# Kernel optimization log

Measured on AMD Instinct MI355X. Metric: run time of the kernel, lower is better.

The kernel has to match this reference:

```python
import jax, jax.numpy as jnp
import numpy as np

H, DH = 16, 64  # heads, dim_head (inner_dim = 1024)
VARIANCE_CONSTANT = 1.0


def setup_inputs() -> dict:
    key = jax.random.key(0)
    ks = jax.random.split(key, 6)
    b, n, m, dim = 8, 4096, 64, 1024
    inner = H * DH
    x = jax.random.normal(ks[0], (b, n, dim), dtype=jnp.float32)
    latents = jax.random.normal(ks[1], (b, m, dim), dtype=jnp.float32)
    mask = jax.random.randint(ks[2], (b, n), 0, 2).astype(bool)  # True = masked out
    sd = 1.0 / np.sqrt(dim)
    Wq = jax.random.normal(ks[3], (inner, dim), dtype=jnp.float32) * sd
    Wkv = jax.random.normal(ks[4], (2 * inner, dim), dtype=jnp.float32) * sd
    Wout = jax.random.normal(ks[5], (dim, inner), dtype=jnp.float32) * sd
    return {"x": x, "latents": latents, "mask": mask, "Wq": Wq, "Wkv": Wkv, "Wout": Wout}


def _split_heads(t):  # b n (h d) -> b h n d
    b, n, _ = t.shape
    return t.reshape(b, n, H, DH).transpose(0, 2, 1, 3)


def reference(x, latents, mask, Wq, Wkv, Wout):
    b, n, dim = x.shape
    scale = DH ** -0.5
    q = latents @ Wq.T                      # b m inner
    k, v = jnp.split(x @ Wkv.T, 2, axis=-1)  # b n inner each
    q = _split_heads(q) * scale             # b h m d
    k = _split_heads(k)                     # b h n d
    v = _split_heads(v)
    sim = jnp.einsum('bhid,bhjd->bhij', q, k)  # b h m n
    max_neg = -jnp.finfo(sim.dtype).max
    sim = jnp.where(mask[:, None, None, :], max_neg, sim)
    sim_new = sim - jax.lax.stop_gradient(sim.max(axis=-1, keepdims=True))
    # cross-query (dim=-2) unbiased variance -> std over latents, shape b h n
    std = jnp.sqrt(jnp.var(sim_new, axis=-2, ddof=1) + 1e-4)
    std = jnp.where(mask[:, None, :], VARIANCE_CONSTANT, std)
    loss_variance = jnp.mean(jax.nn.relu(VARIANCE_CONSTANT - std))
    attn = jax.nn.softmax(sim_new, axis=-1)
    out = jnp.einsum('bhij,bhjd->bhid', attn, v)         # b h m d
    out = out.transpose(0, 2, 1, 3).reshape(b, -1, H * DH)  # b m inner
    out = out @ Wout.T                                    # b m dim
    return out, loss_variance
```

## Files before the change

### kernel.cpp

```cpp
#include <hip/hip_runtime.h>


using u16 = unsigned short;
typedef short bf16x8_t __attribute__((ext_vector_type(8)));
typedef float f32x4_t __attribute__((ext_vector_type(4)));

__device__ __forceinline__ u16 f2bf(float f) {
    union { float f; unsigned u; } v; v.f = f;
    unsigned r = v.u + 0x7fffu + ((v.u >> 16) & 1u);
    return (u16)(r >> 16);
}

template <typename T> __device__ __forceinline__ T cvt_out(float v);
template <> __device__ __forceinline__ float cvt_out<float>(float v) { return v; }
template <> __device__ __forceinline__ u16   cvt_out<u16>(float v)   { return f2bf(v); }

__device__ __forceinline__ void cp16(const void* g, void* l) {
    __builtin_amdgcn_global_load_lds((const __attribute__((address_space(1))) unsigned int*)g,
                                     (__attribute__((address_space(3))) unsigned int*)l, 16, 0, 0);
}

__global__ void cvt_all(const float* __restrict__ x, const float* __restrict__ lat,
                        const float* __restrict__ wq, const float* __restrict__ wkv,
                        const float* __restrict__ wout,
                        u16* __restrict__ xb, u16* __restrict__ latb,
                        u16* __restrict__ wqb, u16* __restrict__ wkvb,
                        u16* __restrict__ woutb) {
    int i = blockIdx.x * 256 + threadIdx.x;
    const float* s; u16* d; int off; float sc = 1.f;
    if (i < 8388608)      { s = x;    d = xb;    off = i; }
    else if (i < 8519680) { s = lat;  d = latb;  off = i - 8388608; }
    else if (i < 8781824) { s = wq;   d = wqb;   off = i - 8519680; sc = 0.125f; }
    else if (i < 9306112) { s = wkv;  d = wkvb;  off = i - 8781824; }
    else if (i < 9568256) { s = wout; d = woutb; off = i - 9306112; }
    else return;
    float4 v = ((const float4*)s)[off];
    ushort4 o;
    o.x = f2bf(v.x * sc); o.y = f2bf(v.y * sc);
    o.z = f2bf(v.z * sc); o.w = f2bf(v.w * sc);
    ((ushort4*)d)[off] = o;
}


__device__ __forceinline__ void stage_half(const u16* __restrict__ G, u16* L,
                                           int grow0, int kt, int tid) {
    const int row8 = tid >> 3;
    const int pcb = tid & 7;
    const int sc = (pcb ^ (row8 & 7)) * 8;
    const int k0 = kt * 64;
    const int wu = (tid >> 6) * 512;
#pragma unroll
    for (int r = 0; r < 2; ++r)
        cp16(G + (size_t)(grow0 + r * 64 + row8) * 1024 + k0 + sc, L + r * 4096 + wu);
}

template <bool E12, bool E34, int WAIT>
__device__ __forceinline__ void tile_phases(
    const u16* At, const u16* Bt,
    const u16* __restrict__ gA, u16* lA, int rowA, int ktA,
    const u16* __restrict__ gB, u16* lB, int rowB, int ktB,
    int wm, int wn, int frow, int pc0, int pc1, int tid,
    f32x4_t (&acc)[8][4]) {
    bf16x8_t aF[4][2], bF[4][2];
#pragma unroll
    for (int i = 0; i < 4; ++i) {
        const u16* p = At + (wm * 128 + i * 16 + frow) * 64;
        aF[i][0] = *(const bf16x8_t*)(p + pc0);
        aF[i][1] = *(const bf16x8_t*)(p + pc1);
    }
#pragma unroll
    for (int j = 0; j < 4; ++j)
        bF[j][0] = *(const bf16x8_t*)(Bt + (wn * 64 + j * 16 + frow) * 64 + pc0);
    if (E12) stage_half(gA, lA, rowA, ktA, tid);
    __builtin_amdgcn_s_barrier();
    asm volatile("s_waitcnt lgkmcnt(0)" ::: "memory");
    __builtin_amdgcn_s_setprio(1);
#pragma unroll
    for (int i = 0; i < 4; ++i)
#pragma unroll
        for (int j = 0; j < 4; ++j)
            acc[i][j] = __builtin_amdgcn_mfma_f32_16x16x32_bf16(aF[i][0], bF[j][0], acc[i][j], 0, 0, 0);
    __builtin_amdgcn_s_setprio(0);
    __builtin_amdgcn_s_barrier();
#pragma unroll
    for (int j = 0; j < 4; ++j)
        bF[j][1] = *(const bf16x8_t*)(Bt + (wn * 64 + j * 16 + frow) * 64 + pc1);
    if (E12) stage_half(gA, lA + 8192, rowA + 128, ktA, tid);
    __builtin_amdgcn_s_barrier();
    asm volatile("s_waitcnt lgkmcnt(0)" ::: "memory");
    __builtin_amdgcn_s_setprio(1);
#pragma unroll
    for (int i = 0; i < 4; ++i)
#pragma unroll
        for (int j = 0; j < 4; ++j)
            acc[i][j] = __builtin_amdgcn_mfma_f32_16x16x32_bf16(aF[i][1], bF[j][1], acc[i][j], 0, 0, 0);
    __builtin_amdgcn_s_setprio(0);
    __builtin_amdgcn_s_barrier();
#pragma unroll
    for (int i = 0; i < 4; ++i) {
        const u16* p = At + (wm * 128 + (i + 4) * 16 + frow) * 64;
        aF[i][0] = *(const bf16x8_t*)(p + pc0);
        aF[i][1] = *(const bf16x8_t*)(p + pc1);
    }
    if (E34) stage_half(gB, lB, rowB, ktB, tid);
    __builtin_amdgcn_s_barrier();
    asm volatile("s_waitcnt lgkmcnt(0)" ::: "memory");
    __builtin_amdgcn_s_setprio(1);
#pragma unroll
    for (int i = 0; i < 4; ++i)
#pragma unroll
        for (int j = 0; j < 4; ++j)
            acc[i + 4][j] = __builtin_amdgcn_mfma_f32_16x16x32_bf16(aF[i][0], bF[j][0], acc[i + 4][j], 0, 0, 0);
    __builtin_amdgcn_s_setprio(0);
    __builtin_amdgcn_s_barrier();
    if (E34) stage_half(gB, lB + 8192, rowB + 128, ktB, tid);
    if (WAIT == 4)      asm volatile("s_waitcnt vmcnt(4)" ::: "memory");
    else if (WAIT == 0) asm volatile("s_waitcnt vmcnt(0)" ::: "memory");
    __builtin_amdgcn_s_barrier();
    __builtin_amdgcn_s_setprio(1);
#pragma unroll
    for (int i = 0; i < 4; ++i)
#pragma unroll
        for (int j = 0; j < 4; ++j)
            acc[i + 4][j] = __builtin_amdgcn_mfma_f32_16x16x32_bf16(aF[i][1], bF[j][1], acc[i + 4][j], 0, 0, 0);
    __builtin_amdgcn_s_setprio(0);
    __builtin_amdgcn_s_barrier();
}

__global__ __launch_bounds__(512, 2) void gemm_kv8(const u16* __restrict__ A,
                                                   const u16* __restrict__ B,
                                                   const u16* __restrict__ Qb,
                                                   const int* __restrict__ mask,
                                                   u16* __restrict__ Kc,
                                                   u16* __restrict__ Vt,
                                                   float* __restrict__ Mg2) {
    __shared__ __align__(16) u16 smem[65536];
    u16* A0 = smem;
    u16* A1 = smem + 16384;
    u16* B0 = smem + 32768;
    u16* B1 = smem + 49152;
    const int tid = threadIdx.x;
    const int wid = tid >> 6, lane = tid & 63;
    const int wm = wid >> 2, wn = wid & 3;
    const int frow = lane & 15, fq = lane >> 4;
    const int pc0 = (fq ^ (frow & 7)) * 8;
    const int pc1 = ((4 + fq) ^ (frow & 7)) * 8;
    const int fid = blockIdx.x;
    const int xcd = fid & 7, l = fid >> 3;
    const int by = xcd * 16 + (l >> 3), bx = l & 7;
    const int bm = by * 256, bn = bx * 256;

    f32x4_t acc[8][4];
#pragma unroll
    for (int i = 0; i < 8; ++i)
#pragma unroll
        for (int j = 0; j < 4; ++j) acc[i][j] = (f32x4_t){0.f, 0.f, 0.f, 0.f};

    stage_half(B, B0, bn, 0, tid);        stage_half(B, B0 + 8192, bn + 128, 0, tid);
    stage_half(A, A0, bm, 0, tid);        stage_half(A, A0 + 8192, bm + 128, 0, tid);
    stage_half(B, B1, bn, 1, tid);        stage_half(B, B1 + 8192, bn + 128, 1, tid);
    asm volatile("s_waitcnt vmcnt(4)" ::: "memory");
    __builtin_amdgcn_s_barrier();

    for (int t = 0; t < 7; ++t) {
        tile_phases<true, true, 4>(A0, B0, A, A1, bm, 2 * t + 1, B, B0, bn, 2 * t + 2,
                                   wm, wn, frow, pc0, pc1, tid, acc);
        tile_phases<true, true, 4>(A1, B1, A, A0, bm, 2 * t + 2, B, B1, bn, 2 * t + 3,
                                   wm, wn, frow, pc0, pc1, tid, acc);
    }
    tile_phases<true, false, 0>(A0, B0, A, A1, bm, 15, B, B1, bn, 0,
                                wm, wn, frow, pc0, pc1, tid, acc);
    tile_phases<false, false, -1>(A1, B1, A, A0, bm, 0, B, B1, bn, 0,
                                  wm, wn, frow, pc0, pc1, tid, acc);

    if (bx < 4) {
        const int bb = bm >> 12, jb = bm & 4095, chunk = by & 15;
#pragma unroll
        for (int i = 0; i < 8; ++i)
#pragma unroll
            for (int j = 0; j < 4; ++j) {
                size_t base = (size_t)(bm + wm * 128 + i * 16 + fq * 4) * 1024 +
                              (bn + wn * 64 + j * 16 + frow);
#pragma unroll
                for (int r = 0; r < 4; ++r)
                    Kc[base + (size_t)r * 1024] = f2bf(acc[i][j][r]);
            }
        u16* Kl = smem;
#pragma unroll
        for (int i = 0; i < 8; ++i)
#pragma unroll
            for (int j = 0; j < 4; ++j) {
                const int cc0 = wn * 64 + j * 16 + frow;
#pragma unroll
                for (int r = 0; r < 4; ++r) {
                    const int jr = wm * 128 + i * 16 + fq * 4 + r;
                    Kl[jr * 256 + (((cc0 >> 3) ^ (jr & 7)) * 8) + (cc0 & 7)] = f2bf(acc[i][j][r]);
                }
            }
        __syncthreads();
        const int hh = wid >> 1, jn = (wid & 1) * 128;
        const int hc = (bx << 2) + hh;
        int mk[8];
#pragma unroll
        for (int jf = 0; jf < 8; ++jf)
            mk[jf] = mask[bb * 4096 + jb + jn + jf * 16 + frow];
        f32x4_t s2[4][8];
#pragma unroll
        for (int i = 0; i < 4; ++i)
#pragma unroll
            for (int jf = 0; jf < 8; ++jf) s2[i][jf] = (f32x4_t){0.f, 0.f, 0.f, 0.f};
#pragma unroll
        for (int ks = 0; ks < 2; ++ks) {
            bf16x8_t aq[4], bk[8];
#pragma unroll
            for (int i = 0; i < 4; ++i)
                aq[i] = *(const bf16x8_t*)(Qb + (size_t)(bb * 64 + i * 16 + frow) * 1024 +
                                           hc * 64 + ks * 32 + fq * 8);
#pragma unroll
            for (int jf = 0; jf < 8; ++jf) {
                const int jr = jn + jf * 16 + frow;
                bk[jf] = *(const bf16x8_t*)(Kl + jr * 256 +
                                            (((hh * 8 + ks * 4 + fq) ^ (jr & 7)) * 8));
            }
#pragma unroll
            for (int i = 0; i < 4; ++i)
#pragma unroll
                for (int jf = 0; jf < 8; ++jf)
                    s2[i][jf] = __builtin_amdgcn_mfma_f32_16x16x32_bf16(aq[i], bk[jf], s2[i][jf], 0, 0, 0);
        }
        float ml[16];
#pragma unroll
        for (int i = 0; i < 16; ++i) ml[i] = -3.0e38f;
#pragma unroll
        for (int jf = 0; jf < 8; ++jf)
            if (!mk[jf])
#pragma unroll
                for (int i = 0; i < 4; ++i)
#pragma unroll
                    for (int r = 0; r < 4; ++r)
                        ml[i * 4 + r] = fmaxf(ml[i * 4 + r], s2[i][jf][r]);
#pragma unroll
        for (int i = 0; i < 16; ++i) {
            float v = ml[i];
            v = fmaxf(v, __shfl_xor(v, 1)); v = fmaxf(v, __shfl_xor(v, 2));
            v = fmaxf(v, __shfl_xor(v, 4)); v = fmaxf(v, __shfl_xor(v, 8));
            ml[i] = v;
        }
        __syncthreads();
        float* Mp = (float*)smem;
        if ((lane & 15) == 0)
#pragma unroll
            for (int i = 0; i < 4; ++i)
#pragma unroll
                for (int r = 0; r < 4; ++r)
                    Mp[wid * 64 + i * 16 + fq * 4 + r] = ml[i * 4 + r];
        __syncthreads();
        if (tid < 256) {
            const int h2 = tid >> 6, m = tid & 63;
            Mg2[((size_t)(bb * 16 + (bx << 2) + h2) * 16 + chunk) * 64 + m] =
                fmaxf(Mp[(2 * h2) * 64 + m], Mp[(2 * h2 + 1) * 64 + m]);
        }
        return;
    }

    const int vb0 = bn - 1024;
    const int b = bm >> 12, jb = bm & 4095;
    u16* Ct = smem;
#pragma unroll
    for (int ph = 0; ph < 2; ++ph) {
        __syncthreads();
        if ((wn >> 1) == ph) {
#pragma unroll
            for (int i = 0; i < 8; ++i)
#pragma unroll
                for (int j = 0; j < 4; ++j) {
                    const int vdl = (wn & 1) * 64 + j * 16 + frow;
                    const int jl = wm * 128 + i * 16 + fq * 4;
                    ushort4 pk;
                    pk.x = f2bf(acc[i][j][0]); pk.y = f2bf(acc[i][j][1]);
                    pk.z = f2bf(acc[i][j][2]); pk.w = f2bf(acc[i][j][3]);
                    *(ushort4*)(Ct + vdl * 264 + jl) = pk;
                }
        }
        __syncthreads();
#pragma unroll
        for (int p = 0; p < 8; ++p) {
            const int idx = p * 512 + tid;
            const int vdl = idx >> 5;
            const int jl = (idx & 31) * 8;
            bf16x8_t v = *(const bf16x8_t*)(Ct + vdl * 264 + jl);
            const int vd = vb0 + ph * 128 + vdl;
            const size_t addr = ((size_t)(b * 16 + (vd >> 6)) * 64 + (vd & 63)) * 4096 + jb + jl;
            *(bf16x8_t*)(Vt + addr) = v;
        }
    }
}

template <typename OutT>
__global__ __launch_bounds__(256) void gemm_bt64(const u16* __restrict__ A,
                                                 const u16* __restrict__ B,
                                                 OutT* __restrict__ C,
                                                 int M, int N, int K) {
    __shared__ __align__(16) u16 As[64 * 64];
    __shared__ __align__(16) u16 Bs[64 * 64];
    const int tid = threadIdx.x;
    const int wid = tid >> 6, lane = tid & 63;
    const int bm = blockIdx.y * 64, bn = blockIdx.x * 64;
    const int srow = lane >> 3;
    const int scol = ((lane & 7) ^ srow) * 8;
    const int frow = lane & 15;
    const int wr = (wid >> 1) * 32, wc = (wid & 1) * 32;

    f32x4_t acc[2][2];
#pragma unroll
    for (int i = 0; i < 2; ++i)
#pragma unroll
        for (int j = 0; j < 2; ++j) acc[i][j] = (f32x4_t){0.f, 0.f, 0.f, 0.f};

    for (int k0 = 0; k0 < K; k0 += 64) {
#pragma unroll
        for (int t = 0; t < 2; ++t) {
            const int c = wid * 2 + t;
            const int r = c * 8 + srow;
            cp16(A + (size_t)(bm + r) * K + k0 + scol, As + c * 512);
            cp16(B + (size_t)(bn + r) * K + k0 + scol, Bs + c * 512);
        }
        __syncthreads();
#pragma unroll
        for (int ks = 0; ks < 2; ++ks) {
            const int grp = (((ks * 4 + (lane >> 4)) ^ (frow & 7)) * 8);
            bf16x8_t af[2], bfv[2];
#pragma unroll
            for (int i = 0; i < 2; ++i) {
                af[i]  = *(const bf16x8_t*)(As + (wr + i * 16 + frow) * 64 + grp);
                bfv[i] = *(const bf16x8_t*)(Bs + (wc + i * 16 + frow) * 64 + grp);
            }
#pragma unroll
            for (int i = 0; i < 2; ++i)
#pragma unroll
                for (int j = 0; j < 2; ++j)
                    acc[i][j] = __builtin_amdgcn_mfma_f32_16x16x32_bf16(af[i], bfv[j], acc[i][j], 0, 0, 0);
        }
        __syncthreads();
    }
    const int cr = (lane >> 4) * 4, cc = lane & 15;
#pragma unroll
    for (int i = 0; i < 2; ++i)
#pragma unroll
        for (int j = 0; j < 2; ++j) {
            size_t base = (size_t)(bm + wr + i * 16 + cr) * N + (bn + wc + j * 16 + cc);
#pragma unroll
            for (int r = 0; r < 4; ++r)
                C[base + (size_t)r * N] = cvt_out<OutT>(acc[i][j][r]);
        }
}

__global__ __launch_bounds__(256, 2) void attn_pv(const u16* __restrict__ q,
                                                  const u16* __restrict__ kbuf,
                                                  const u16* __restrict__ vtbuf,
                                                  const int* __restrict__ mask,
                                                  const float* __restrict__ Mg,
                                                  float* __restrict__ Opart,
                                                  float* __restrict__ Rpart,
                                                  float* __restrict__ loss) {
    const int c = blockIdx.x & 3, bh = blockIdx.x >> 2, b = bh >> 4, h = bh & 15;
    const int tid = threadIdx.x, wid = tid >> 6, lane = tid & 63;
    const int frow = lane & 15, cr = (lane >> 4) * 4;
    const int srow = lane >> 3, scol = ((lane & 7) ^ srow) * 8;

    __shared__ __align__(16) u16 qs[64 * 64];
    __shared__ __align__(16) u16 wbuf[4][2][4096];
    __shared__ float Mrow[64];
    __shared__ float RpS[4][64];
    __shared__ float lossP[4];

    const size_t kbase  = (size_t)b * 4096 * 1024 + (size_t)h * 64;
    const size_t vtbase = (size_t)bh * 64 * 4096;
    const int cb = c * 1024;
    u16* Kw = &wbuf[wid][0][0];
    u16* Vw = &wbuf[wid][1][0];

#pragma unroll
    for (int t = 0; t < 2; ++t) {
        int cq = wid * 2 + t;
        int r = cq * 8 + srow;
        cp16(q + (size_t)(b * 64 + r) * 1024 + h * 64 + scol, qs + cq * 512);
    }
    if (tid < 64) {
        float m = -3.0e38f;
#pragma unroll
        for (int cc = 0; cc < 16; ++cc) m = fmaxf(m, Mg[(size_t)(bh * 16 + cc) * 64 + tid]);
        Mrow[tid] = m;
    }
    __syncthreads();

    f32x4_t oacc[4][4];
#pragma unroll
    for (int i = 0; i < 4; ++i)
#pragma unroll
        for (int j = 0; j < 4; ++j) oacc[i][j] = (f32x4_t){0.f, 0.f, 0.f, 0.f};
    float rloc[16];
#pragma unroll
    for (int i = 0; i < 16; ++i) rloc[i] = 0.f;
    float lossacc = 0.f;

    for (int sc = 0; sc < 4; ++sc) {
        const int j0 = cb + (sc * 4 + wid) * 64;
#pragma unroll
        for (int t = 0; t < 8; ++t) {
            int r = t * 8 + srow;
            cp16(kbuf + kbase + (size_t)(j0 + r) * 1024 + scol, Kw + t * 512);
        }
#pragma unroll
        for (int t = 0; t < 8; ++t) {
            int d = t * 8 + srow;
            cp16(vtbuf + vtbase + (size_t)d * 4096 + j0 + scol, Vw + t * 512);
        }
        __builtin_amdgcn_s_waitcnt(0);

        f32x4_t sacc[4][4];
#pragma unroll
        for (int i = 0; i < 4; ++i)
#pragma unroll
            for (int j = 0; j < 4; ++j) sacc[i][j] = (f32x4_t){0.f, 0.f, 0.f, 0.f};
#pragma unroll
        for (int ks2 = 0; ks2 < 2; ++ks2) {
            const int grp = (((ks2 * 4 + (lane >> 4)) ^ (frow & 7)) * 8);
            bf16x8_t af[4], bfv[4];
#pragma unroll
            for (int i = 0; i < 4; ++i) {
                af[i]  = *(const bf16x8_t*)(qs + (i * 16 + frow) * 64 + grp);
                bfv[i] = *(const bf16x8_t*)(Kw + (i * 16 + frow) * 64 + grp);
            }
#pragma unroll
            for (int i = 0; i < 4; ++i)
#pragma unroll
                for (int j = 0; j < 4; ++j)
                    sacc[i][j] = __builtin_amdgcn_mfma_f32_16x16x32_bf16(af[i], bfv[j], sacc[i][j], 0, 0, 0);
        }

#pragma unroll
        for (int nt = 0; nt < 4; ++nt) {
            const int jl = nt * 16 + frow;
            const bool msk = mask[b * 4096 + j0 + jl] != 0;
            const int jh = jl >> 3, jlo = jl & 7;
            float c1 = 0.f, c2 = 0.f;
#pragma unroll
            for (int mt = 0; mt < 4; ++mt) {
#pragma unroll
                for (int r = 0; r < 4; ++r) {
                    const int row = mt * 16 + cr + r;
                    const float t = sacc[mt][nt][r] - Mrow[row];
                    const float p = msk ? 0.f : __expf(t);
                    rloc[mt * 4 + r] += p;
                    c1 += msk ? 0.f : t;
                    c2 += msk ? 0.f : t * t;
                    Kw[row * 64 + ((jh ^ (row & 7)) * 8) + jlo] = f2bf(p);
                }
            }
            c1 += __shfl_xor(c1, 16); c1 += __shfl_xor(c1, 32);
            c2 += __shfl_xor(c2, 16); c2 += __shfl_xor(c2, 32);
            if (lane < 16 && !msk) {
                const float var = (c2 - c1 * c1 * (1.f / 64.f)) * (1.f / 63.f);
                lossacc += fmaxf(1.f - sqrtf(var + 1e-4f), 0.f);
            }
        }
#pragma unroll
        for (int ks2 = 0; ks2 < 2; ++ks2) {
            const int grp = (((ks2 * 4 + (lane >> 4)) ^ (frow & 7)) * 8);
            bf16x8_t pa[4], vb[4];
#pragma unroll
            for (int i = 0; i < 4; ++i) {
                pa[i] = *(const bf16x8_t*)(Kw + (i * 16 + frow) * 64 + grp);
                vb[i] = *(const bf16x8_t*)(Vw + (i * 16 + frow) * 64 + grp);
            }
#pragma unroll
            for (int i = 0; i < 4; ++i)
#pragma unroll
                for (int j = 0; j < 4; ++j)
                    oacc[i][j] = __builtin_amdgcn_mfma_f32_16x16x32_bf16(pa[i], vb[j], oacc[i][j], 0, 0, 0);
        }
    }

    float* Osw = (float*)(&wbuf[0][0][0]) + wid * 4096;
#pragma unroll
    for (int i = 0; i < 4; ++i)
#pragma unroll
        for (int j = 0; j < 4; ++j)
#pragma unroll
            for (int r = 0; r < 4; ++r)
                Osw[(i * 16 + cr + r) * 64 + j * 16 + frow] = oacc[i][j][r];

#pragma unroll
    for (int i = 0; i < 16; ++i) {
        float v = rloc[i];
        v += __shfl_xor(v, 1); v += __shfl_xor(v, 2);
        v += __shfl_xor(v, 4); v += __shfl_xor(v, 8);
        rloc[i] = v;
    }
    if ((lane & 15) == 0) {
#pragma unroll
        for (int mt = 0; mt < 4; ++mt)
#pragma unroll
            for (int r = 0; r < 4; ++r)
                RpS[wid][mt * 16 + cr + r] = rloc[mt * 4 + r];
    }
    float v = lossacc;
    v += __shfl_xor(v, 1); v += __shfl_xor(v, 2); v += __shfl_xor(v, 4);
    v += __shfl_xor(v, 8); v += __shfl_xor(v, 16); v += __shfl_xor(v, 32);
    if (lane == 0) lossP[wid] = v;
    __syncthreads();

    const float4* Ob4 = (const float4*)(&wbuf[0][0][0]);
    const size_t ob = (size_t)(bh * 4 + c) * 4096;
#pragma unroll
    for (int p = 0; p < 4; ++p) {
        const int e = tid + p * 256;
        float4 s0 = Ob4[e];
        float4 s1 = Ob4[e + 1024];
        float4 s2 = Ob4[e + 2048];
        float4 s3 = Ob4[e + 3072];
        float4 o;
        o.x = s0.x + s1.x + s2.x + s3.x;
        o.y = s0.y + s1.y + s2.y + s3.y;
        o.z = s0.z + s1.z + s2.z + s3.z;
        o.w = s0.w + s1.w + s2.w + s3.w;
        ((float4*)(Opart + ob))[e] = o;
    }
    if (tid < 64)
        Rpart[(size_t)(bh * 4 + c) * 64 + tid] =
            RpS[0][tid] + RpS[1][tid] + RpS[2][tid] + RpS[3][tid];
    if (tid == 0)
        atomicAdd(loss, (lossP[0] + lossP[1] + lossP[2] + lossP[3]) * (1.f / 524288.f));
}

__global__ __launch_bounds__(256) void attn_fin(const float* __restrict__ Opart,
                                                const float* __restrict__ Rpart,
                                                u16* __restrict__ ao) {
    const int bh = blockIdx.x, b = bh >> 4, h = bh & 15;
    const int tid = threadIdx.x;
    __shared__ float Rt[64];
    if (tid < 64) {
        float r = 0.f;
#pragma unroll
        for (int cc = 0; cc < 4; ++cc) r += Rpart[(size_t)(bh * 4 + cc) * 64 + tid];
        Rt[tid] = r;
    }
    __syncthreads();
    for (int e = tid; e < 4096; e += 256) {
        float o = 0.f;
#pragma unroll
        for (int cc = 0; cc < 4; ++cc) o += Opart[(size_t)(bh * 4 + cc) * 4096 + e];
        const int row = e >> 6, d = e & 63;
        ao[(size_t)(b * 64 + row) * 1024 + h * 64 + d] = f2bf(o / Rt[row]);
    }
}

extern "C" void kernel_launch(void* const* d_in, const int* in_sizes, int n_in,
                              void* d_out, int out_size, void* d_ws, size_t ws_size,
                              hipStream_t stream) {
    const float* x    = (const float*)d_in[0];
    const float* lat  = (const float*)d_in[1];
    const int*   mask = (const int*)d_in[2];
    const float* Wq   = (const float*)d_in[3];
    const float* Wkv  = (const float*)d_in[4];
    const float* Wout = (const float*)d_in[5];
    float* out = (float*)d_out;

    char* ws = (char*)d_ws;
    u16* x_bf    = (u16*)(ws);
    u16* kbuf    = (u16*)(ws + 67108864);
    u16* vtbuf   = (u16*)(ws + 134217728);
    u16* wq_bf   = (u16*)(ws + 201326592);
    u16* wkv_bf  = (u16*)(ws + 203423744);
    u16* wout_bf = (u16*)(ws + 207618048);
    u16* lat_bf  = (u16*)(ws + 209715200);
    u16* q_bf    = (u16*)(ws + 210763776);
    u16* ao_bf   = (u16*)(ws + 211812352);
    float* Mg    = (float*)(ws + 201326592);
    float* Opart = (float*)(ws + 1048576);
    float* Rpart = (float*)(ws + 1048576 + 8388608);

    hipMemsetAsync(out + 524288, 0, 4, stream);

    cvt_all<<<37376, 256, 0, stream>>>(x, lat, Wq, Wkv, Wout,
                                       x_bf, lat_bf, wq_bf, wkv_bf, wout_bf);

    dim3 blk(256);
    gemm_bt64<u16><<<dim3(16, 8), blk, 0, stream>>>(lat_bf, wq_bf, q_bf, 512, 1024, 1024);
    gemm_kv8<<<dim3(1024), dim3(512), 0, stream>>>(x_bf, wkv_bf, q_bf, mask, kbuf, vtbuf, Mg);
    attn_pv<<<512, blk, 0, stream>>>(q_bf, kbuf, vtbuf, mask, Mg, Opart, Rpart, out + 524288);
    attn_fin<<<128, blk, 0, stream>>>(Opart, Rpart, ao_bf);
    gemm_bt64<float><<<dim3(16, 8), blk, 0, stream>>>(ao_bf, wout_bf, out, 512, 1024, 1024);
}
```

Baseline: 437.0 us.

## Split attn_pv across more blocks, read K/V directly, coalesce K stores

In the KV GEMM, K is now written from the swizzled LDS tile with 16-byte coalesced stores instead of scattered 2-byte stores. attn_pv doubles its grid to 8 sequence chunks per head and drops the LDS staging of K and V, reading MFMA operands straight from global memory. Each wave writes its own partial output, and attn_fin reduces 32 partials with float4 loads. The LDS footprint shrinks so three blocks can fit per CU, in exchange for more global traffic for partials and uncached operand loads.

```diff
diff --git a/kernel.cpp b/kernel.cpp
--- a/kernel.cpp
+++ b/kernel.cpp
@@ -175,16 +175,6 @@
 
     if (bx < 4) {
         const int bb = bm >> 12, jb = bm & 4095, chunk = by & 15;
-#pragma unroll
-        for (int i = 0; i < 8; ++i)
-#pragma unroll
-            for (int j = 0; j < 4; ++j) {
-                size_t base = (size_t)(bm + wm * 128 + i * 16 + fq * 4) * 1024 +
-                              (bn + wn * 64 + j * 16 + frow);
-#pragma unroll
-                for (int r = 0; r < 4; ++r)
-                    Kc[base + (size_t)r * 1024] = f2bf(acc[i][j][r]);
-            }
         u16* Kl = smem;
 #pragma unroll
         for (int i = 0; i < 8; ++i)
@@ -198,6 +188,13 @@
                 }
             }
         __syncthreads();
+#pragma unroll
+        for (int p = 0; p < 16; ++p) {
+            const int idx = p * 512 + tid;
+            const int jr = idx >> 5, cb = idx & 31;
+            bf16x8_t v = *(const bf16x8_t*)(Kl + jr * 256 + ((cb ^ (jr & 7)) * 8));
+            *(bf16x8_t*)(Kc + (size_t)(bm + jr) * 1024 + bn + cb * 8) = v;
+        }
         const int hh = wid >> 1, jn = (wid & 1) * 128;
         const int hc = (bx << 2) + hh;
         int mk[8];
@@ -355,7 +352,7 @@
         }
 }
 
-__global__ __launch_bounds__(256, 2) void attn_pv(const u16* __restrict__ q,
+__global__ __launch_bounds__(256, 3) void attn_pv(const u16* __restrict__ q,
                                                   const u16* __restrict__ kbuf,
                                                   const u16* __restrict__ vtbuf,
                                                   const int* __restrict__ mask,
@@ -363,22 +360,21 @@
                                                   float* __restrict__ Opart,
                                                   float* __restrict__ Rpart,
                                                   float* __restrict__ loss) {
-    const int c = blockIdx.x & 3, bh = blockIdx.x >> 2, b = bh >> 4, h = bh & 15;
+    const int c = blockIdx.x & 7, bh = blockIdx.x >> 3, b = bh >> 4, h = bh & 15;
     const int tid = threadIdx.x, wid = tid >> 6, lane = tid & 63;
-    const int frow = lane & 15, cr = (lane >> 4) * 4;
+    const int frow = lane & 15, fq = lane >> 4, cr = fq * 4;
     const int srow = lane >> 3, scol = ((lane & 7) ^ srow) * 8;
 
     __shared__ __align__(16) u16 qs[64 * 64];
-    __shared__ __align__(16) u16 wbuf[4][2][4096];
+    __shared__ __align__(16) u16 Pw[4][4096];
     __shared__ float Mrow[64];
     __shared__ float RpS[4][64];
     __shared__ float lossP[4];
 
     const size_t kbase  = (size_t)b * 4096 * 1024 + (size_t)h * 64;
     const size_t vtbase = (size_t)bh * 64 * 4096;
-    const int cb = c * 1024;
-    u16* Kw = &wbuf[wid][0][0];
-    u16* Vw = &wbuf[wid][1][0];
+    const int cb = c * 512;
+    u16* Pl = &Pw[wid][0];
 
 #pragma unroll
     for (int t = 0; t < 2; ++t) {
@@ -404,44 +400,30 @@
     for (int i = 0; i < 16; ++i) rloc[i] = 0.f;
     float lossacc = 0.f;
 
-    for (int sc = 0; sc < 4; ++sc) {
+    for (int sc = 0; sc < 2; ++sc) {
         const int j0 = cb + (sc * 4 + wid) * 64;
-#pragma unroll
-        for (int t = 0; t < 8; ++t) {
-            int r = t * 8 + srow;
-            cp16(kbuf + kbase + (size_t)(j0 + r) * 1024 + scol, Kw + t * 512);
-        }
-#pragma unroll
-        for (int t = 0; t < 8; ++t) {
-            int d = t * 8 + srow;
-            cp16(vtbuf + vtbase + (size_t)d * 4096 + j0 + scol, Vw + t * 512);
-        }
-        __builtin_amdgcn_s_waitcnt(0);
-
-        f32x4_t sacc[4][4];
-#pragma unroll
-        for (int i = 0; i < 4; ++i)
-#pragma unroll
-            for (int j = 0; j < 4; ++j) sacc[i][j] = (f32x4_t){0.f, 0.f, 0.f, 0.f};
+        bf16x8_t af[4][2];
 #pragma unroll
         for (int ks2 = 0; ks2 < 2; ++ks2) {
-            const int grp = (((ks2 * 4 + (lane >> 4)) ^ (frow & 7)) * 8);
-            bf16x8_t af[4], bfv[4];
-#pragma unroll
-            for (int i = 0; i < 4; ++i) {
-                af[i]  = *(const bf16x8_t*)(qs + (i * 16 + frow) * 64 + grp);
-                bfv[i] = *(const bf16x8_t*)(Kw + (i * 16 + frow) * 64 + grp);
-            }
+            const int grp = (((ks2 * 4 + fq) ^ (frow & 7)) * 8);
 #pragma unroll
             for (int i = 0; i < 4; ++i)
-#pragma unroll
-                for (int j = 0; j < 4; ++j)
-                    sacc[i][j] = __builtin_amdgcn_mfma_f32_16x16x32_bf16(af[i], bfv[j], sacc[i][j], 0, 0, 0);
-        }
-
-#pragma unroll
-        for (int nt = 0; nt < 4; ++nt) {
-            const int jl = nt * 16 + frow;
+                af[i][ks2] = *(const bf16x8_t*)(qs + (i * 16 + frow) * 64 + grp);
+        }
+#pragma unroll
+        for (int jcol = 0; jcol < 4; ++jcol) {
+            f32x4_t sj[4];
+#pragma unroll
+            for (int i = 0; i < 4; ++i) sj[i] = (f32x4_t){0.f, 0.f, 0.f, 0.f};
+#pragma unroll
+            for (int ks2 = 0; ks2 < 2; ++ks2) {
+                bf16x8_t bk = *(const bf16x8_t*)(kbuf + kbase +
+                    (size_t)(j0 + jcol * 16 + frow) * 1024 + ks2 * 32 + fq * 8);
+#pragma unroll
+                for (int i = 0; i < 4; ++i)
+                    sj[i] = __builtin_amdgcn_mfma_f32_16x16x32_bf16(af[i][ks2], bk, sj[i], 0, 0, 0);
+            }
+            const int jl = jcol * 16 + frow;
             const bool msk = mask[b * 4096 + j0 + jl] != 0;
             const int jh = jl >> 3, jlo = jl & 7;
             float c1 = 0.f, c2 = 0.f;
@@ -450,12 +432,12 @@
 #pragma unroll
                 for (int r = 0; r < 4; ++r) {
                     const int row = mt * 16 + cr + r;
-                    const float t = sacc[mt][nt][r] - Mrow[row];
+                    const float t = sj[mt][r] - Mrow[row];
                     const float p = msk ? 0.f : __expf(t);
                     rloc[mt * 4 + r] += p;
                     c1 += msk ? 0.f : t;
                     c2 += msk ? 0.f : t * t;
-                    Kw[row * 64 + ((jh ^ (row & 7)) * 8) + jlo] = f2bf(p);
+                    Pl[row * 64 + ((jh ^ (row & 7)) * 8) + jlo] = f2bf(p);
                 }
             }
             c1 += __shfl_xor(c1, 16); c1 += __shfl_xor(c1, 32);
@@ -467,12 +449,13 @@
         }
 #pragma unroll
         for (int ks2 = 0; ks2 < 2; ++ks2) {
-            const int grp = (((ks2 * 4 + (lane >> 4)) ^ (frow & 7)) * 8);
+            const int grp = (((ks2 * 4 + fq) ^ (frow & 7)) * 8);
             bf16x8_t pa[4], vb[4];
 #pragma unroll
             for (int i = 0; i < 4; ++i) {
-                pa[i] = *(const bf16x8_t*)(Kw + (i * 16 + frow) * 64 + grp);
-                vb[i] = *(const bf16x8_t*)(Vw + (i * 16 + frow) * 64 + grp);
+                pa[i] = *(const bf16x8_t*)(Pl + (i * 16 + frow) * 64 + grp);
+                vb[i] = *(const bf16x8_t*)(vtbuf + vtbase +
+                        (size_t)(i * 16 + frow) * 4096 + j0 + ks2 * 32 + fq * 8);
             }
 #pragma unroll
             for (int i = 0; i < 4; ++i)
@@ -482,14 +465,14 @@
         }
     }
 
-    float* Osw = (float*)(&wbuf[0][0][0]) + wid * 4096;
+    const size_t ob = ((size_t)((bh * 8 + c) * 4) + wid) * 4096;
 #pragma unroll
     for (int i = 0; i < 4; ++i)
 #pragma unroll
         for (int j = 0; j < 4; ++j)
 #pragma unroll
             for (int r = 0; r < 4; ++r)
-                Osw[(i * 16 + cr + r) * 64 + j * 16 + frow] = oacc[i][j][r];
+                Opart[ob + (size_t)(i * 16 + cr + r) * 64 + j * 16 + frow] = oacc[i][j][r];
 
 #pragma unroll
     for (int i = 0; i < 16; ++i) {
@@ -510,25 +493,8 @@
     v += __shfl_xor(v, 8); v += __shfl_xor(v, 16); v += __shfl_xor(v, 32);
     if (lane == 0) lossP[wid] = v;
     __syncthreads();
-
-    const float4* Ob4 = (const float4*)(&wbuf[0][0][0]);
-    const size_t ob = (size_t)(bh * 4 + c) * 4096;
-#pragma unroll
-    for (int p = 0; p < 4; ++p) {
-        const int e = tid + p * 256;
-        float4 s0 = Ob4[e];
-        float4 s1 = Ob4[e + 1024];
-        float4 s2 = Ob4[e + 2048];
-        float4 s3 = Ob4[e + 3072];
-        float4 o;
-        o.x = s0.x + s1.x + s2.x + s3.x;
-        o.y = s0.y + s1.y + s2.y + s3.y;
-        o.z = s0.z + s1.z + s2.z + s3.z;
-        o.w = s0.w + s1.w + s2.w + s3.w;
-        ((float4*)(Opart + ob))[e] = o;
-    }
     if (tid < 64)
-        Rpart[(size_t)(bh * 4 + c) * 64 + tid] =
+        Rpart[(size_t)(bh * 8 + c) * 64 + tid] =
             RpS[0][tid] + RpS[1][tid] + RpS[2][tid] + RpS[3][tid];
     if (tid == 0)
         atomicAdd(loss, (lossP[0] + lossP[1] + lossP[2] + lossP[3]) * (1.f / 524288.f));
@@ -543,16 +509,23 @@
     if (tid < 64) {
         float r = 0.f;
 #pragma unroll
-        for (int cc = 0; cc < 4; ++cc) r += Rpart[(size_t)(bh * 4 + cc) * 64 + tid];
+        for (int cc = 0; cc < 8; ++cc) r += Rpart[(size_t)(bh * 8 + cc) * 64 + tid];
         Rt[tid] = r;
     }
     __syncthreads();
-    for (int e = tid; e < 4096; e += 256) {
-        float o = 0.f;
-#pragma unroll
-        for (int cc = 0; cc < 4; ++cc) o += Opart[(size_t)(bh * 4 + cc) * 4096 + e];
-        const int row = e >> 6, d = e & 63;
-        ao[(size_t)(b * 64 + row) * 1024 + h * 64 + d] = f2bf(o / Rt[row]);
+    for (int e4 = tid; e4 < 1024; e4 += 256) {
+        float4 o = make_float4(0.f, 0.f, 0.f, 0.f);
+#pragma unroll
+        for (int p = 0; p < 32; ++p) {
+            float4 s = ((const float4*)(Opart + ((size_t)(bh * 32 + p)) * 4096))[e4];
+            o.x += s.x; o.y += s.y; o.z += s.z; o.w += s.w;
+        }
+        const int e = e4 * 4, row = e >> 6, d = e & 63;
+        const float rinv = 1.f / Rt[row];
+        ushort4 pk;
+        pk.x = f2bf(o.x * rinv); pk.y = f2bf(o.y * rinv);
+        pk.z = f2bf(o.z * rinv); pk.w = f2bf(o.w * rinv);
+        *(ushort4*)(ao + (size_t)(b * 64 + row) * 1024 + h * 64 + d) = pk;
     }
 }
 
@@ -578,8 +551,8 @@
     u16* q_bf    = (u16*)(ws + 210763776);
     u16* ao_bf   = (u16*)(ws + 211812352);
     float* Mg    = (float*)(ws + 201326592);
-    float* Opart = (float*)(ws + 1048576);
-    float* Rpart = (float*)(ws + 1048576 + 8388608);
+    float* Rpart = (float*)(ws + 201326592 + 524288);
+    float* Opart = (float*)(ws);
 
     hipMemsetAsync(out + 524288, 0, 4, stream);
 
@@ -589,7 +562,7 @@
     dim3 blk(256);
     gemm_bt64<u16><<<dim3(16, 8), blk, 0, stream>>>(lat_bf, wq_bf, q_bf, 512, 1024, 1024);
     gemm_kv8<<<dim3(1024), dim3(512), 0, stream>>>(x_bf, wkv_bf, q_bf, mask, kbuf, vtbuf, Mg);
-    attn_pv<<<512, blk, 0, stream>>>(q_bf, kbuf, vtbuf, mask, Mg, Opart, Rpart, out + 524288);
+    attn_pv<<<1024, blk, 0, stream>>>(q_bf, kbuf, vtbuf, mask, Mg, Opart, Rpart, out + 524288);
     attn_fin<<<128, blk, 0, stream>>>(Opart, Rpart, ao_bf);
     gemm_bt64<float><<<dim3(16, 8), blk, 0, stream>>>(ao_bf, wout_bf, out, 512, 1024, 1024);
 }
```

Measured after the change: 619.9 us. 41.9% more time.
